# Kernel optimization log

Measured on AMD Instinct MI355X. Metric: run time of the kernel, lower is better.

Reference implementation:

```python
import jax, jax.numpy as jnp
import numpy as np

DIM = 64
HID = 32  # dim * 1/2
P = 4     # patch_size

def _conv1x1(x, w):
    # x: [B,C,H,W], w: [O,C] -> [B,O,H,W]
    return jnp.einsum('oc,bchw->bohw', w, x)

def _dwconv3x3(x, w):
    # depthwise 3x3, padding 1. x: [B,C,H,W], w: [C,1,3,3]
    return jax.lax.conv_general_dilated(
        x, w, window_strides=(1, 1), padding=((1, 1), (1, 1)),
        dimension_numbers=('NCHW', 'OIHW', 'NCHW'),
        feature_group_count=x.shape[1])

def setup_inputs() -> dict:
    key = jax.random.key(0)
    k1, k2, k3, k4 = jax.random.split(key, 4)
    B, H, W = 4, 512, 512
    x = jax.random.normal(k1, (B, DIM, H, W), dtype=jnp.float32)
    w_in1 = jax.random.normal(k2, (2 * HID, DIM), dtype=jnp.float32) * 0.05
    w_dw = jax.random.normal(k3, (2 * HID, 1, 3, 3), dtype=jnp.float32) * 0.1
    w_in2 = jax.random.normal(k4, (DIM, HID), dtype=jnp.float32) * 0.05
    w_freq = jnp.ones((DIM, 1, 1, P, P // 2 + 1), dtype=jnp.float32)
    return {'x': x, 'w_in1': w_in1, 'w_dw': w_dw, 'w_in2': w_in2, 'w_freq': w_freq}

def reference(x, w_in1, w_dw, w_in2, w_freq):
    shortcut = x
    y = _dwconv3x3(_conv1x1(x, w_in1), w_dw)          # [B,2*HID,H,W]
    y1, y2 = jnp.split(y, 2, axis=1)
    y = jax.nn.gelu(y1, approximate=False) * y2       # [B,HID,H,W]
    y = _conv1x1(y, w_in2)                            # [B,DIM,H,W]
    b, c, h, w = y.shape
    h_n = (P - h % P) % P
    w_n = (P - w % P) % P
    if h_n or w_n:
        y = jnp.pad(y, ((0, 0), (0, 0), (0, h_n), (0, w_n)), mode='reflect')
    hp, wp = y.shape[2] // P, y.shape[3] // P
    # [B,C,hp,P,wp,P] -> [B,C,hp,wp,P,P]
    yp = y.reshape(b, c, hp, P, wp, P).transpose(0, 1, 2, 4, 3, 5)
    yf = jnp.fft.rfft2(yp)                            # [B,C,hp,wp,P,P//2+1] complex
    yf = w_freq * yf                                  # w_freq broadcasts over (C,1,1,P,P//2+1)
    yp = jnp.fft.irfft2(yf, s=(P, P))
    y = yp.transpose(0, 1, 2, 4, 3, 5).reshape(b, c, hp * P, wp * P)
    y = y[:, :, :h, :w]
    return y + shortcut
```

## Files before the change

### kernel.cpp

```cpp
#include <hip/hip_runtime.h>
#include <hip/hip_fp16.h>
#include <math.h>

#define DIMC 64
#define HIDC 32
#define IMH 512
#define IMW 512
#define TW 32
#define TH 16
#define HW 34
#define HH 18
#define NPIX (HW*HH)
#define NPIXP 624
#define NCHUNK 39
#define PLANE (IMH*IMW)

#define IDOFF 0
#define W1OFF 16
#define W2OFF 2064
#define PWOFF 3088

typedef _Float16 half8  __attribute__((ext_vector_type(8)));
typedef __fp16   fp16x2 __attribute__((ext_vector_type(2)));
typedef float f32x4     __attribute__((ext_vector_type(4)));
typedef unsigned int uint;

union U4H8 { uint4 u; half8 h; };

static __device__ __forceinline__ uint pkrtz(float a, float b) {
    union { fp16x2 h; uint u; } x;
    x.h = __builtin_amdgcn_cvt_pkrtz(a, b);
    return x.u;
}
static __device__ __forceinline__ float lo16f(uint u) {
    union { uint u; _Float16 h[2]; } x; x.u = u; return (float)x.h[0];
}
static __device__ __forceinline__ float hi16f(uint u) {
    union { uint u; _Float16 h[2]; } x; x.u = u; return (float)x.h[1];
}
static __device__ __forceinline__ uint pkfma(uint w, uint t, uint acc) {
    union { uint u; __half2 h; } W, T, A;
    W.u = w; T.u = t; A.u = acc;
    A.h = __hfma2(W.h, T.h, A.h);
    return A.u;
}

static __device__ __forceinline__ float gelu_f(float u) {
    const float z  = fabsf(u) * 0.70710678118654752f;
    const float t  = __builtin_amdgcn_rcpf(fmaf(0.3275911f, z, 1.0f));
    const float e  = __builtin_amdgcn_exp2f(-z * z * 1.4426950408889634f);
    float p = fmaf(t, 1.061405429f, -1.453152027f);
    p = fmaf(t, p, 1.421413741f);
    p = fmaf(t, p, -0.284496736f);
    p = fmaf(t, p, 0.254829592f);
    p = p * t;
    const float erf_abs = fmaf(-p, e, 1.0f);
    const float erfv = copysignf(erf_abs, u);
    return 0.5f * u * (1.0f + erfv);
}

__global__ __launch_bounds__(256)
void ffn_prep(const float* __restrict__ w1, const float* __restrict__ wdw,
              const float* __restrict__ w2, const float* __restrict__ wf,
              uint* __restrict__ ws)
{
    __shared__ int sid;
    const int tid = threadIdx.x;
    if (tid == 0) sid = 1;
    __syncthreads();
    bool ok = true;
    for (int i = tid; i < DIMC * 12; i += 256) ok = ok && (wf[i] == 1.0f);
    if (!ok) atomicAnd(&sid, 0);
    for (int i = tid; i < 2048; i += 256) ws[W1OFF + i] = pkrtz(w1[2*i], w1[2*i+1]);
    for (int i = tid; i < 1024; i += 256) ws[W2OFF + i] = pkrtz(w2[2*i], w2[2*i+1]);
    for (int i = tid; i < 288; i += 256) {
        const int k = i >> 5, ch = i & 31;
        ws[PWOFF + i] = pkrtz(wdw[ch*9 + k], wdw[(ch + HIDC)*9 + k]);
    }
    __syncthreads();
    if (tid == 0) ws[IDOFF] = (uint)sid;
}

__global__ __launch_bounds__(512, 4)
void ffn_main(const float* __restrict__ x,
              const uint*  __restrict__ ws,
              const float* __restrict__ wf,
              float* __restrict__ out)
{
    __shared__ uint ts[NPIXP * 32];

    const int tid = threadIdx.x;
    const int bid = ((blockIdx.x & 7) << 8) + (blockIdx.x >> 3);
    const int b  = bid >> 9;
    const int tr = bid & 511;
    const int ty = tr >> 4, tx = tr & 15;
    const int oy = ty * TH, ox = tx * TW;

    const float* xb = x + (size_t)b * DIMC * PLANE;

    for (int p = tid; p < NPIXP; p += 512) {
        const int hy = p / HW, hx = p - hy * HW;
        const int gy = oy + hy - 1, gx = ox + hx - 1;
        const uint base = (uint)p << 5, sw = ((uint)p & 7) << 2;
        if (p >= NPIX || (unsigned)gy >= IMH || (unsigned)gx >= IMW) {
            #pragma unroll
            for (int g = 0; g < 8; ++g) {
                uint4 z = {0u, 0u, 0u, 0u};
                *reinterpret_cast<uint4*>(&ts[base + (((uint)g << 2) ^ sw)]) = z;
            }
        } else {
            const float* xp = xb + (size_t)gy * IMW + gx;
            #pragma unroll
            for (int g = 0; g < 8; ++g) {
                float f[8];
                #pragma unroll
                for (int i = 0; i < 8; ++i) f[i] = xp[(size_t)(g * 8 + i) * PLANE];
                uint4 o;
                o.x = pkrtz(f[0], f[1]); o.y = pkrtz(f[2], f[3]);
                o.z = pkrtz(f[4], f[5]); o.w = pkrtz(f[6], f[7]);
                *reinterpret_cast<uint4*>(&ts[base + (((uint)g << 2) ^ sw)]) = o;
            }
        }
    }

    const int lane = tid & 63, wid = tid >> 6;
    const int l15 = lane & 15, lg = lane >> 4;

    half8 afrag1[4][2];
    const uint4* w1v = reinterpret_cast<const uint4*>(ws + W1OFF);
    #pragma unroll
    for (int mt = 0; mt < 4; ++mt)
        #pragma unroll
        for (int ks = 0; ks < 2; ++ks) {
            U4H8 u; u.u = w1v[(mt*16 + l15)*8 + ks*4 + lg];
            afrag1[mt][ks] = u.h;
        }
    half8 afrag2[4];
    const uint4* w2v = reinterpret_cast<const uint4*>(ws + W2OFF);
    #pragma unroll
    for (int mt = 0; mt < 4; ++mt) { U4H8 u; u.u = w2v[(mt*16 + l15)*4 + lg]; afrag2[mt] = u.h; }

    const uint ident = ws[IDOFF];
    __syncthreads();

    uint xs[4][4][2];
    #pragma unroll
    for (int cc = 0; cc < 4; ++cc) {
        const int px = wid*64 + cc*16 + l15;
        const int h  = ((px >> 5) + 1) * HW + (px & 31) + 1;
        const uint base = (uint)h << 5, sw = ((uint)h & 7) << 2;
        #pragma unroll
        for (int mt = 0; mt < 4; ++mt) {
            const uint a = base + (((uint)(mt*8 + lg*2)) ^ sw);
            xs[cc][mt][0] = ts[a];
            xs[cc][mt][1] = ts[a + 1];
        }
    }
    __syncthreads();

    for (int chunk = wid; chunk < NCHUNK; chunk += 8) {
        const uint px = (uint)(chunk*16 + l15);
        const uint base = px << 5, sw = (px & 7) << 2;
        f32x4 acc[4];
        #pragma unroll
        for (int mt = 0; mt < 4; ++mt) acc[mt] = (f32x4)0.0f;
        #pragma unroll
        for (int ks = 0; ks < 2; ++ks) {
            U4H8 u; u.u = *reinterpret_cast<const uint4*>(&ts[base + (((uint)(ks*16 + lg*4)) ^ sw)]);
            #pragma unroll
            for (int mt = 0; mt < 4; ++mt)
                acc[mt] = __builtin_amdgcn_mfma_f32_16x16x32_f16(afrag1[mt][ks], u.h, acc[mt], 0, 0, 0);
        }
        #pragma unroll
        for (int mt = 0; mt < 2; ++mt) {
            uint4 o;
            o.x = pkrtz(acc[mt][0], acc[mt+2][0]);
            o.y = pkrtz(acc[mt][1], acc[mt+2][1]);
            o.z = pkrtz(acc[mt][2], acc[mt+2][2]);
            o.w = pkrtz(acc[mt][3], acc[mt+2][3]);
            *reinterpret_cast<uint4*>(&ts[base + (((uint)(mt*16 + lg*4)) ^ sw)]) = o;
        }
    }
    __syncthreads();

    const int li = tid >> 5, lj = tid & 31;
    uint acc2[32];
    #pragma unroll
    for (int c = 0; c < 32; ++c) acc2[c] = 0u;
    #pragma unroll
    for (int k = 0; k < 9; ++k) {
        const int di = k / 3, dj = k - di * 3;
        const uint hpx = (uint)((li + di) * HW + (lj + dj));
        const uint base = hpx << 5, sw = (hpx & 7) << 2;
        const uint4* pwv = reinterpret_cast<const uint4*>(ws + PWOFF + k*32);
        #pragma unroll
        for (int g = 0; g < 8; ++g) {
            const uint4 wv = pwv[g];
            const uint4 tv = *reinterpret_cast<const uint4*>(&ts[base + (((uint)g << 2) ^ sw)]);
            acc2[g*4+0] = pkfma(wv.x, tv.x, acc2[g*4+0]);
            acc2[g*4+1] = pkfma(wv.y, tv.y, acc2[g*4+1]);
            acc2[g*4+2] = pkfma(wv.z, tv.z, acc2[g*4+2]);
            acc2[g*4+3] = pkfma(wv.w, tv.w, acc2[g*4+3]);
        }
    }
    uint4 vo[4];
    #pragma unroll
    for (int gg = 0; gg < 4; ++gg) {
        uint o[4];
        #pragma unroll
        for (int q = 0; q < 4; ++q) {
            const int c2 = gg*4 + q;
            const uint wa = acc2[2*c2], wb = acc2[2*c2 + 1];
            const float v0 = gelu_f(lo16f(wa)) * hi16f(wa);
            const float v1 = gelu_f(lo16f(wb)) * hi16f(wb);
            o[q] = pkrtz(v0, v1);
        }
        vo[gg].x = o[0]; vo[gg].y = o[1]; vo[gg].z = o[2]; vo[gg].w = o[3];
    }
    __syncthreads();
    {
        const uint vb = (uint)tid << 4, swv = ((uint)tid & 3) << 2;
        #pragma unroll
        for (int gg = 0; gg < 4; ++gg)
            *reinterpret_cast<uint4*>(&ts[vb + (((uint)gg << 2) ^ swv)]) = vo[gg];
    }
    __syncthreads();

    float* ob = out + (size_t)b * DIMC * PLANE;
    if (ident) {
        #pragma unroll
        for (int cc = 0; cc < 4; ++cc) {
            const uint px = (uint)(wid*64 + cc*16 + l15);
            U4H8 u; u.u = *reinterpret_cast<const uint4*>(&ts[(px << 4) + ((((uint)lg ^ (px & 3))) << 2)]);
            const size_t pix = (size_t)(oy + (int)(px >> 5)) * IMW + (ox + (int)(px & 31));
            float* op = ob + pix;
            #pragma unroll
            for (int mt = 0; mt < 4; ++mt) {
                f32x4 a = __builtin_amdgcn_mfma_f32_16x16x32_f16(afrag2[mt], u.h, (f32x4)0.0f, 0, 0, 0);
                #pragma unroll
                for (int r = 0; r < 4; ++r) {
                    const int ch = mt*16 + lg*4 + r;
                    const uint xw = xs[cc][mt][r >> 1];
                    const float xv = (r & 1) ? hi16f(xw) : lo16f(xw);
                    op[(size_t)ch * PLANE] = a[r] + xv;
                }
            }
        }
    } else {
        float* ys = reinterpret_cast<float*>(ts + 8192);
        for (int mt = 0; mt < 4; ++mt) {
            __syncthreads();
            #pragma unroll
            for (int cc = 0; cc < 4; ++cc) {
                const uint px = (uint)(wid*64 + cc*16 + l15);
                U4H8 u; u.u = *reinterpret_cast<const uint4*>(&ts[(px << 4) + ((((uint)lg ^ (px & 3))) << 2)]);
                f32x4 a = __builtin_amdgcn_mfma_f32_16x16x32_f16(afrag2[mt], u.h, (f32x4)0.0f, 0, 0, 0);
                #pragma unroll
                for (int r = 0; r < 4; ++r)
                    ys[(lg*4 + r) * 520 + (int)px] = a[r];
            }
            __syncthreads();
            {
                const int chl = tid >> 5;
                const int ch  = mt*16 + chl;
                const int pt  = tid & 31;
                const int pi = (pt >> 3) * 4, pj = (pt & 7) * 4;
                float yv[4][4];
                #pragma unroll
                for (int a = 0; a < 4; ++a)
                    #pragma unroll
                    for (int c = 0; c < 4; ++c)
                        yv[a][c] = ys[chl * 520 + (pi + a) * TW + (pj + c)];
                float Cr[4][4], Ci[4][4];
                #pragma unroll
                for (int j = 0; j < 4; ++j) {
                    const float s02 = yv[0][j] + yv[2][j], d02 = yv[0][j] - yv[2][j];
                    const float s13 = yv[1][j] + yv[3][j], d13 = yv[1][j] - yv[3][j];
                    Cr[0][j] = s02 + s13; Ci[0][j] = 0.0f;
                    Cr[1][j] = d02;       Ci[1][j] = -d13;
                    Cr[2][j] = s02 - s13; Ci[2][j] = 0.0f;
                    Cr[3][j] = d02;       Ci[3][j] = d13;
                }
                float Zr[4][3], Zi[4][3];
                #pragma unroll
                for (int u = 0; u < 4; ++u) {
                    const float r0 = Cr[u][0], r1 = Cr[u][1], r2 = Cr[u][2], r3 = Cr[u][3];
                    const float i0 = Ci[u][0], i1 = Ci[u][1], i2 = Ci[u][2], i3 = Ci[u][3];
                    Zr[u][0] = r0 + r1 + r2 + r3;     Zi[u][0] = i0 + i1 + i2 + i3;
                    Zr[u][1] = (r0 - r2) + (i1 - i3); Zi[u][1] = (i0 - i2) - (r1 - r3);
                    Zr[u][2] = r0 - r1 + r2 - r3;     Zi[u][2] = i0 - i1 + i2 - i3;
                    #pragma unroll
                    for (int vv = 0; vv < 3; ++vv) {
                        const float m = wf[ch * 12 + u * 3 + vv];
                        Zr[u][vv] *= m; Zi[u][vv] *= m;
                    }
                }
                float Ar[4][3], Ai[4][3];
                #pragma unroll
                for (int vv = 0; vv < 3; ++vv) {
                    const float r0 = Zr[0][vv], r1 = Zr[1][vv], r2 = Zr[2][vv], r3 = Zr[3][vv];
                    const float i0 = Zi[0][vv], i1 = Zi[1][vv], i2 = Zi[2][vv], i3 = Zi[3][vv];
                    Ar[0][vv] = r0 + r1 + r2 + r3;     Ai[0][vv] = i0 + i1 + i2 + i3;
                    Ar[1][vv] = (r0 - r2) - (i1 - i3); Ai[1][vv] = (i0 - i2) + (r1 - r3);
                    Ar[2][vv] = r0 - r1 + r2 - r3;     Ai[2][vv] = i0 - i1 + i2 - i3;
                    Ar[3][vv] = (r0 - r2) + (i1 - i3); Ai[3][vv] = (i0 - i2) - (r1 - r3);
                }
                const float* xc = xb + (size_t)ch * PLANE;
                float*       oc = ob + (size_t)ch * PLANE;
                #pragma unroll
                for (int a = 0; a < 4; ++a) {
                    const float A0 = Ar[a][0], A1r = Ar[a][1], A2 = Ar[a][2];
                    const float B1i = Ai[a][1];
                    float res[4];
                    res[0] = (A0 + 2.0f * A1r + A2) * 0.0625f;
                    res[1] = (A0 - 2.0f * B1i - A2) * 0.0625f;
                    res[2] = (A0 - 2.0f * A1r + A2) * 0.0625f;
                    res[3] = (A0 + 2.0f * B1i - A2) * 0.0625f;
                    #pragma unroll
                    for (int c = 0; c < 4; ++c) {
                        const size_t pix = (size_t)(oy + pi + a) * IMW + (ox + pj + c);
                        oc[pix] = res[c] + xc[pix];
                    }
                }
            }
        }
    }
}

extern "C" void kernel_launch(void* const* d_in, const int* in_sizes, int n_in,
                              void* d_out, int out_size, void* d_ws, size_t ws_size,
                              hipStream_t stream) {
    (void)in_sizes; (void)n_in; (void)ws_size; (void)out_size;
    const float* x   = (const float*)d_in[0];
    const float* w1  = (const float*)d_in[1];
    const float* wdw = (const float*)d_in[2];
    const float* w2  = (const float*)d_in[3];
    const float* wf  = (const float*)d_in[4];
    float* out = (float*)d_out;
    uint* ws = (uint*)d_ws;

    ffn_prep<<<1, 256, 0, stream>>>(w1, wdw, w2, wf, ws);
    const int blocks = 4 * (IMH / TH) * (IMW / TW);
    ffn_main<<<blocks, 512, 0, stream>>>(x, ws, wf, out);
}
```

Baseline: 191.0 us.

## Halve tile height, split depthwise channels across thread halves, raise occupancy

```diff
diff --git a/kernel.cpp b/kernel.cpp
--- a/kernel.cpp
+++ b/kernel.cpp
@@ -7,12 +7,13 @@
 #define IMH 512
 #define IMW 512
 #define TW 32
-#define TH 16
+#define TH 8
 #define HW 34
-#define HH 18
+#define HH 10
 #define NPIX (HW*HH)
-#define NPIXP 624
-#define NCHUNK 39
+#define NPIXP 352
+#define NCHUNK 22
+#define VSTR 20
 #define PLANE (IMH*IMW)
 
 #define IDOFF 0
@@ -81,7 +82,24 @@
     if (tid == 0) ws[IDOFF] = (uint)sid;
 }
 
-__global__ __launch_bounds__(512, 4)
+static __device__ __forceinline__ void stage_px(uint* ts, const float* xp, uint p) {
+    const uint base = p << 5, sw = (p & 7) << 2;
+    #pragma unroll
+    for (int h = 0; h < 2; ++h) {
+        float f[32];
+        #pragma unroll
+        for (int i = 0; i < 32; ++i) f[i] = xp[(size_t)(h*32 + i) * PLANE];
+        #pragma unroll
+        for (int g = 0; g < 4; ++g) {
+            uint4 o;
+            o.x = pkrtz(f[g*8+0], f[g*8+1]); o.y = pkrtz(f[g*8+2], f[g*8+3]);
+            o.z = pkrtz(f[g*8+4], f[g*8+5]); o.w = pkrtz(f[g*8+6], f[g*8+7]);
+            *reinterpret_cast<uint4*>(&ts[base + (((uint)((h*4 + g) << 2)) ^ sw)]) = o;
+        }
+    }
+}
+
+__global__ __launch_bounds__(512, 6)
 void ffn_main(const float* __restrict__ x,
               const uint*  __restrict__ ws,
               const float* __restrict__ wf,
@@ -90,41 +108,34 @@
     __shared__ uint ts[NPIXP * 32];
 
     const int tid = threadIdx.x;
-    const int bid = ((blockIdx.x & 7) << 8) + (blockIdx.x >> 3);
-    const int b  = bid >> 9;
-    const int tr = bid & 511;
+    const int bid = ((blockIdx.x & 7) << 9) + (blockIdx.x >> 3);
+    const int b  = bid >> 10;
+    const int tr = bid & 1023;
     const int ty = tr >> 4, tx = tr & 15;
     const int oy = ty * TH, ox = tx * TW;
 
     const float* xb = x + (size_t)b * DIMC * PLANE;
 
-    for (int p = tid; p < NPIXP; p += 512) {
+    if (tid < NPIXP) {
+        const int p = tid;
         const int hy = p / HW, hx = p - hy * HW;
         const int gy = oy + hy - 1, gx = ox + hx - 1;
-        const uint base = (uint)p << 5, sw = ((uint)p & 7) << 2;
         if (p >= NPIX || (unsigned)gy >= IMH || (unsigned)gx >= IMW) {
+            const uint base = (uint)p << 5, sw = ((uint)p & 7) << 2;
             #pragma unroll
             for (int g = 0; g < 8; ++g) {
                 uint4 z = {0u, 0u, 0u, 0u};
-                *reinterpret_cast<uint4*>(&ts[base + (((uint)g << 2) ^ sw)]) = z;
+                *reinterpret_cast<uint4*>(&ts[base + (((uint)(g << 2)) ^ sw)]) = z;
             }
         } else {
-            const float* xp = xb + (size_t)gy * IMW + gx;
-            #pragma unroll
-            for (int g = 0; g < 8; ++g) {
-                float f[8];
-                #pragma unroll
-                for (int i = 0; i < 8; ++i) f[i] = xp[(size_t)(g * 8 + i) * PLANE];
-                uint4 o;
-                o.x = pkrtz(f[0], f[1]); o.y = pkrtz(f[2], f[3]);
-                o.z = pkrtz(f[4], f[5]); o.w = pkrtz(f[6], f[7]);
-                *reinterpret_cast<uint4*>(&ts[base + (((uint)g << 2) ^ sw)]) = o;
-            }
+            stage_px(ts, xb + (size_t)gy * IMW + gx, (uint)p);
         }
     }
 
     const int lane = tid & 63, wid = tid >> 6;
     const int l15 = lane & 15, lg = lane >> 4;
+    const int ph = tid >> 8, pq = tid & 255;
+    const int li = pq >> 5, lj = pq & 31;
 
     half8 afrag1[4][2];
     const uint4* w1v = reinterpret_cast<const uint4*>(ws + W1OFF);
@@ -143,10 +154,10 @@
     const uint ident = ws[IDOFF];
     __syncthreads();
 
-    uint xs[4][4][2];
-    #pragma unroll
-    for (int cc = 0; cc < 4; ++cc) {
-        const int px = wid*64 + cc*16 + l15;
+    uint xs[2][4][2];
+    #pragma unroll
+    for (int cc = 0; cc < 2; ++cc) {
+        const int px = (wid*2 + cc)*16 + l15;
         const int h  = ((px >> 5) + 1) * HW + (px & 31) + 1;
         const uint base = (uint)h << 5, sw = ((uint)h & 7) << 2;
         #pragma unroll
@@ -183,10 +194,9 @@
     }
     __syncthreads();
 
-    const int li = tid >> 5, lj = tid & 31;
-    uint acc2[32];
-    #pragma unroll
-    for (int c = 0; c < 32; ++c) acc2[c] = 0u;
+    uint acc2[16];
+    #pragma unroll
+    for (int c = 0; c < 16; ++c) acc2[c] = 0u;
     #pragma unroll
     for (int k = 0; k < 9; ++k) {
         const int di = k / 3, dj = k - di * 3;
@@ -194,44 +204,40 @@
         const uint base = hpx << 5, sw = (hpx & 7) << 2;
         const uint4* pwv = reinterpret_cast<const uint4*>(ws + PWOFF + k*32);
         #pragma unroll
-        for (int g = 0; g < 8; ++g) {
+        for (int gg = 0; gg < 4; ++gg) {
+            const int g = ph*4 + gg;
             const uint4 wv = pwv[g];
-            const uint4 tv = *reinterpret_cast<const uint4*>(&ts[base + (((uint)g << 2) ^ sw)]);
-            acc2[g*4+0] = pkfma(wv.x, tv.x, acc2[g*4+0]);
-            acc2[g*4+1] = pkfma(wv.y, tv.y, acc2[g*4+1]);
-            acc2[g*4+2] = pkfma(wv.z, tv.z, acc2[g*4+2]);
-            acc2[g*4+3] = pkfma(wv.w, tv.w, acc2[g*4+3]);
-        }
-    }
-    uint4 vo[4];
-    #pragma unroll
-    for (int gg = 0; gg < 4; ++gg) {
-        uint o[4];
-        #pragma unroll
-        for (int q = 0; q < 4; ++q) {
-            const int c2 = gg*4 + q;
-            const uint wa = acc2[2*c2], wb = acc2[2*c2 + 1];
-            const float v0 = gelu_f(lo16f(wa)) * hi16f(wa);
-            const float v1 = gelu_f(lo16f(wb)) * hi16f(wb);
-            o[q] = pkrtz(v0, v1);
-        }
-        vo[gg].x = o[0]; vo[gg].y = o[1]; vo[gg].z = o[2]; vo[gg].w = o[3];
+            const uint4 tv = *reinterpret_cast<const uint4*>(&ts[base + (((uint)(g << 2)) ^ sw)]);
+            acc2[gg*4+0] = pkfma(wv.x, tv.x, acc2[gg*4+0]);
+            acc2[gg*4+1] = pkfma(wv.y, tv.y, acc2[gg*4+1]);
+            acc2[gg*4+2] = pkfma(wv.z, tv.z, acc2[gg*4+2]);
+            acc2[gg*4+3] = pkfma(wv.w, tv.w, acc2[gg*4+3]);
+        }
+    }
+    uint vv[8];
+    #pragma unroll
+    for (int q = 0; q < 8; ++q) {
+        const uint wa = acc2[2*q], wb = acc2[2*q + 1];
+        const float v0 = gelu_f(lo16f(wa)) * hi16f(wa);
+        const float v1 = gelu_f(lo16f(wb)) * hi16f(wb);
+        vv[q] = pkrtz(v0, v1);
     }
     __syncthreads();
     {
-        const uint vb = (uint)tid << 4, swv = ((uint)tid & 3) << 2;
-        #pragma unroll
-        for (int gg = 0; gg < 4; ++gg)
-            *reinterpret_cast<uint4*>(&ts[vb + (((uint)gg << 2) ^ swv)]) = vo[gg];
+        uint4 o0 = {vv[0], vv[1], vv[2], vv[3]};
+        uint4 o1 = {vv[4], vv[5], vv[6], vv[7]};
+        const uint vb = (uint)pq * VSTR + (uint)(ph*8);
+        *reinterpret_cast<uint4*>(&ts[vb])     = o0;
+        *reinterpret_cast<uint4*>(&ts[vb + 4]) = o1;
     }
     __syncthreads();
 
     float* ob = out + (size_t)b * DIMC * PLANE;
     if (ident) {
         #pragma unroll
-        for (int cc = 0; cc < 4; ++cc) {
-            const uint px = (uint)(wid*64 + cc*16 + l15);
-            U4H8 u; u.u = *reinterpret_cast<const uint4*>(&ts[(px << 4) + ((((uint)lg ^ (px & 3))) << 2)]);
+        for (int cc = 0; cc < 2; ++cc) {
+            const uint px = (uint)((wid*2 + cc)*16 + l15);
+            U4H8 u; u.u = *reinterpret_cast<const uint4*>(&ts[px * VSTR + (uint)(lg*4)]);
             const size_t pix = (size_t)(oy + (int)(px >> 5)) * IMW + (ox + (int)(px & 31));
             float* op = ob + pix;
             #pragma unroll
@@ -247,30 +253,30 @@
             }
         }
     } else {
-        float* ys = reinterpret_cast<float*>(ts + 8192);
+        float* ys = reinterpret_cast<float*>(ts + 5120);
         for (int mt = 0; mt < 4; ++mt) {
             __syncthreads();
             #pragma unroll
-            for (int cc = 0; cc < 4; ++cc) {
-                const uint px = (uint)(wid*64 + cc*16 + l15);
-                U4H8 u; u.u = *reinterpret_cast<const uint4*>(&ts[(px << 4) + ((((uint)lg ^ (px & 3))) << 2)]);
+            for (int cc = 0; cc < 2; ++cc) {
+                const uint px = (uint)((wid*2 + cc)*16 + l15);
+                U4H8 u; u.u = *reinterpret_cast<const uint4*>(&ts[px * VSTR + (uint)(lg*4)]);
                 f32x4 a = __builtin_amdgcn_mfma_f32_16x16x32_f16(afrag2[mt], u.h, (f32x4)0.0f, 0, 0, 0);
                 #pragma unroll
                 for (int r = 0; r < 4; ++r)
-                    ys[(lg*4 + r) * 520 + (int)px] = a[r];
+                    ys[(lg*4 + r) * 264 + (int)px] = a[r];
             }
             __syncthreads();
-            {
-                const int chl = tid >> 5;
+            if (tid < 256) {
+                const int chl = tid >> 4;
                 const int ch  = mt*16 + chl;
-                const int pt  = tid & 31;
+                const int pt  = tid & 15;
                 const int pi = (pt >> 3) * 4, pj = (pt & 7) * 4;
                 float yv[4][4];
                 #pragma unroll
                 for (int a = 0; a < 4; ++a)
                     #pragma unroll
                     for (int c = 0; c < 4; ++c)
-                        yv[a][c] = ys[chl * 520 + (pi + a) * TW + (pj + c)];
+                        yv[a][c] = ys[chl * 264 + (pi + a) * TW + (pj + c)];
                 float Cr[4][4], Ci[4][4];
                 #pragma unroll
                 for (int j = 0; j < 4; ++j) {
@@ -290,20 +296,20 @@
                     Zr[u][1] = (r0 - r2) + (i1 - i3); Zi[u][1] = (i0 - i2) - (r1 - r3);
                     Zr[u][2] = r0 - r1 + r2 - r3;     Zi[u][2] = i0 - i1 + i2 - i3;
                     #pragma unroll
-                    for (int vv = 0; vv < 3; ++vv) {
-                        const float m = wf[ch * 12 + u * 3 + vv];
-                        Zr[u][vv] *= m; Zi[u][vv] *= m;
+                    for (int vq = 0; vq < 3; ++vq) {
+                        const float m = wf[ch * 12 + u * 3 + vq];
+                        Zr[u][vq] *= m; Zi[u][vq] *= m;
                     }
                 }
                 float Ar[4][3], Ai[4][3];
                 #pragma unroll
-                for (int vv = 0; vv < 3; ++vv) {
-                    const float r0 = Zr[0][vv], r1 = Zr[1][vv], r2 = Zr[2][vv], r3 = Zr[3][vv];
-                    const float i0 = Zi[0][vv], i1 = Zi[1][vv], i2 = Zi[2][vv], i3 = Zi[3][vv];
-                    Ar[0][vv] = r0 + r1 + r2 + r3;     Ai[0][vv] = i0 + i1 + i2 + i3;
-                    Ar[1][vv] = (r0 - r2) - (i1 - i3); Ai[1][vv] = (i0 - i2) + (r1 - r3);
-                    Ar[2][vv] = r0 - r1 + r2 - r3;     Ai[2][vv] = i0 - i1 + i2 - i3;
-                    Ar[3][vv] = (r0 - r2) + (i1 - i3); Ai[3][vv] = (i0 - i2) - (r1 - r3);
+                for (int vq = 0; vq < 3; ++vq) {
+                    const float r0 = Zr[0][vq], r1 = Zr[1][vq], r2 = Zr[2][vq], r3 = Zr[3][vq];
+                    const float i0 = Zi[0][vq], i1 = Zi[1][vq], i2 = Zi[2][vq], i3 = Zi[3][vq];
+                    Ar[0][vq] = r0 + r1 + r2 + r3;     Ai[0][vq] = i0 + i1 + i2 + i3;
+                    Ar[1][vq] = (r0 - r2) - (i1 - i3); Ai[1][vq] = (i0 - i2) + (r1 - r3);
+                    Ar[2][vq] = r0 - r1 + r2 - r3;     Ai[2][vq] = i0 - i1 + i2 - i3;
+                    Ar[3][vq] = (r0 - r2) + (i1 - i3); Ai[3][vq] = (i0 - i2) - (r1 - r3);
                 }
                 const float* xc = xb + (size_t)ch * PLANE;
                 float*       oc = ob + (size_t)ch * PLANE;
```

New measurement: 258.6 us. +35.4%, slower.
